# Kernel optimization log

Hardware: AMD Instinct MI355X
Metric: run time of the kernel (lower is better)

Reference implementation:

```python
import jax, jax.numpy as jnp
import numpy as np

CLIP_LEN = 8      # == num_frame
NUM_NODES = 7     # == group_size
NUM_BASIC = 1024
NUM_MIXED = 8192
T = 2 * CLIP_LEN - 1          # 15 temporal offsets
N = 1 + NUM_NODES * CLIP_LEN  # 57 graph size


def setup_inputs() -> dict:
    key = jax.random.key(0)
    k1, k2, k3, k4 = jax.random.split(key, 4)
    mat = jax.random.normal(k1, (NUM_BASIC, NUM_NODES, NUM_NODES), dtype=jnp.float32)
    temp_extent = jax.random.normal(k2, (NUM_BASIC, T), dtype=jnp.float32)
    # nn.Linear(num_basic, num_mixed): weight [out,in], bias [out]
    W = jax.random.normal(k3, (NUM_MIXED, NUM_BASIC), dtype=jnp.float32) * (1.0 / np.sqrt(NUM_BASIC))
    b = jax.random.normal(k4, (NUM_MIXED,), dtype=jnp.float32) * 0.01
    return {"mat": mat, "temp_extent": temp_extent, "W": W, "b": b}


def reference(mat, temp_extent, W, b):
    n, cl = NUM_NODES, CLIP_LEN
    Hb = mat.shape[0]
    te = jax.nn.sigmoid(temp_extent) + 1.0                      # [Hb, T]
    x = jnp.einsum('ht,hnm->htmn', te, mat)                     # [Hb, T, n, n]
    x = jax.nn.relu(x)
    x = jnp.transpose(x, (1, 2, 3, 0)).reshape(T * n, n, Hb)    # (t m) n h
    y = x @ W.T + b                                             # [(t m), n, Hm]
    y = jax.nn.relu(jnp.transpose(y, (2, 1, 0)))                # [Hm, n, T*n]
    Hm = y.shape[0]
    # vectorized version of the per-frame slice-write loop:
    # frame i reads cols n*(cl-1-i) : n*(2*cl-1-i) of y
    starts = n * (cl - 1 - jnp.arange(cl))                      # [cl]
    idx = starts[:, None] + jnp.arange(n * cl)[None, :]         # [cl, n*cl]
    blocks = y[:, :, idx]                                       # [Hm, n, cl, n*cl]
    blocks = jnp.transpose(blocks, (0, 2, 1, 3)).reshape(Hm, n * cl, n * cl)
    base = jnp.zeros((Hm, N, N), dtype=y.dtype)
    base = base.at[:, 0::7, 0::7].set(1.0)                      # person-node anchors
    mixed = base.at[:, 1:, 1:].set(blocks)                      # [Hm, N, N]
    # degree normalization D^{-1/2} A D^{-1/2} (row sums, clamped at 1)
    d = jnp.clip(mixed.sum(axis=2), 1.0, None) ** -0.5          # [Hm, N]
    ret = d[:, :, None] * mixed * d[:, None, :]
    return ret
```

## Files before the change

### kernel.cpp

```cpp
#include <hip/hip_runtime.h>
#include <hip/hip_bf16.h>

#define HB 1024
#define HM 8192
#define NR 735
#define NPAD 768
#define NOUT 57
#define KSPLIT 2
#define JB 4
#define YS 737

typedef __attribute__((ext_vector_type(8))) _Float16 half8;
typedef __attribute__((ext_vector_type(4))) _Float16 half4v;
typedef __attribute__((ext_vector_type(4))) float floatx4;

__global__ __launch_bounds__(256) void prep_x2_kernel(
    const float* __restrict__ mat, const float* __restrict__ tex,
    _Float16* __restrict__ Xh) {
  const int r = blockIdx.x;
  const int n = r % 7;
  const int tm = r / 7;
  const int m = tm % 7;
  const int t = tm / 7;
#pragma unroll
  for (int i = 0; i < 4; ++i) {
    const int h = i * 256 + threadIdx.x;
    float v = 0.f;
    if (r < NR) {
      const float mv = mat[h * 49 + n * 7 + m];
      const float te = 1.f / (1.f + expf(-tex[h * 15 + t])) + 1.f;
      v = te * mv;
      v = v > 0.f ? v : 0.f;
    }
    Xh[r * HB + h] = (_Float16)v;
  }
}

__global__ __launch_bounds__(256, 3) void gemm_kernel(
    const float* __restrict__ W,
    const _Float16* __restrict__ Xh,
    _Float16* __restrict__ Yp) {
  __shared__ __align__(16) _Float16 As[128 * 32];
  __shared__ __align__(16) _Float16 Bs[128 * 32];

  const int tid = threadIdx.x;
  const int lane = tid & 63;
  const int wave = tid >> 6;
  const int bn = blockIdx.x;
  const int bm = blockIdx.y;
  const int ks = blockIdx.z;
  const int wm = (wave >> 1) * 64;
  const int wn = (wave & 1) * 64;

  floatx4 acc[4][4] = {};

  const int brow = lane >> 2;
  const int bkh = (lane & 3) * 8;
  const size_t bbase = (size_t)(bn * 128) * HB;

  const int arow = tid >> 3;
  const int acol = (tid & 7) * 4;
  const float* const Wbase = W + (size_t)(bm * 128) * HB;

  const int mrow = lane & 15;
  const int quad = lane >> 4;

  const int kbeg = ks * (HB / KSPLIT);
  for (int kk = 0; kk < HB / KSPLIT; kk += 32) {
    const int k0 = kbeg + kk;
#pragma unroll
    for (int it = 0; it < 2; ++it) {
      const int chunk = wave * 2 + it;
      __builtin_amdgcn_global_load_lds(
          (const __attribute__((address_space(1))) void*)(
              Xh + bbase + (size_t)(chunk * 16 + brow) * HB + k0 + bkh),
          (__attribute__((address_space(3))) void*)(Bs + chunk * 512), 16, 0, 0);
    }
#pragma unroll
    for (int it = 0; it < 4; ++it) {
      const int r = it * 32 + arow;
      const float4 w4 = *(const float4*)(Wbase + (size_t)r * HB + k0 + acol);
      half4v h4;
      h4.x = (_Float16)w4.x;
      h4.y = (_Float16)w4.y;
      h4.z = (_Float16)w4.z;
      h4.w = (_Float16)w4.w;
      *(half4v*)(As + r * 32 + acol) = h4;
    }
    __syncthreads();

    half8 af[4], bf[4];
#pragma unroll
    for (int i = 0; i < 4; ++i) {
      af[i] = *(const half8*)(As + (wm + i * 16 + mrow) * 32 + quad * 8);
      bf[i] = *(const half8*)(Bs + (wn + i * 16 + mrow) * 32 + quad * 8);
    }
#pragma unroll
    for (int i = 0; i < 4; ++i)
#pragma unroll
      for (int j = 0; j < 4; ++j)
        acc[i][j] = __builtin_amdgcn_mfma_f32_16x16x32_f16(af[i], bf[j], acc[i][j], 0, 0, 0);
    __syncthreads();
  }

  _Float16* const Yk = Yp + (size_t)ks * HM * NPAD;
#pragma unroll
  for (int i = 0; i < 4; ++i) {
#pragma unroll
    for (int j = 0; j < 4; ++j) {
#pragma unroll
      for (int reg = 0; reg < 4; ++reg) {
        const int grow = bm * 128 + wm + i * 16 + quad * 4 + reg;
        const int gcol = bn * 128 + wn + j * 16 + mrow;
        Yk[(size_t)grow * NPAD + gcol] = (_Float16)acc[i][j][reg];
      }
    }
  }
}

__global__ __launch_bounds__(256) void epilogue_kernel(
    const _Float16* __restrict__ Yp, const float* __restrict__ bias,
    float* __restrict__ out) {
  const int tid = threadIdx.x;
  const int j0 = blockIdx.x * JB;
  __shared__ float ly[JB][YS];
  __shared__ float dd[JB][NOUT];

#pragma unroll
  for (int jj = 0; jj < JB; ++jj) {
    const _Float16* y0 = Yp + (size_t)(j0 + jj) * NPAD;
    const _Float16* y1 = Yp + (size_t)(HM + j0 + jj) * NPAD;
    const float bj = bias[j0 + jj];
    for (int i = tid; i < NR; i += 256) {
      float v = (float)y0[i] + (float)y1[i] + bj;
      ly[jj][i] = v > 0.f ? v : 0.f;
    }
  }
  __syncthreads();

  if (tid < JB * NOUT) {
    const int jj = tid / NOUT;
    const int r = tid % NOUT;
    float s;
    if (r == 0) {
      s = 9.f;
    } else {
      const int c = (r - 1) / 7;
      const int n = (r - 1) % 7;
      const int base = 7 * (7 - c);
      s = (n == 6) ? 1.f : 0.f;
#pragma unroll
      for (int p = 0; p < 56; ++p) s += ly[jj][(base + p) * 7 + n];
    }
    s = s < 1.f ? 1.f : s;
    dd[jj][r] = rsqrtf(s);
  }
  __syncthreads();

  float4* const o4 = (float4*)(out + (size_t)j0 * (NOUT * NOUT));
  for (int idx = tid; idx < NOUT * NOUT; idx += 256) {
    float4 v4;
#pragma unroll
    for (int e = 0; e < 4; ++e) {
      const int g = idx * 4 + e;
      const int jj = g / (NOUT * NOUT);
      const int i = g % (NOUT * NOUT);
      const int r = i / NOUT;
      const int q = i % NOUT;
      float v;
      if (r == 0) {
        v = (q % 7 == 0) ? dd[jj][0] * dd[jj][q] : 0.f;
      } else {
        const int c = (r - 1) / 7;
        const int n = (r - 1) % 7;
        if (q == 0)
          v = (n == 6) ? dd[jj][r] * dd[jj][0] : 0.f;
        else
          v = dd[jj][r] * ly[jj][(7 * (7 - c) + q - 1) * 7 + n] * dd[jj][q];
      }
      ((float*)&v4)[e] = v;
    }
    o4[idx] = v4;
  }
}

extern "C" void kernel_launch(void* const* d_in, const int* in_sizes, int n_in,
                              void* d_out, int out_size, void* d_ws, size_t ws_size,
                              hipStream_t stream) {
  const float* mat = (const float*)d_in[0];
  const float* tex = (const float*)d_in[1];
  const float* W = (const float*)d_in[2];
  const float* b = (const float*)d_in[3];
  float* out = (float*)d_out;

  char* ws = (char*)d_ws;
  _Float16* Xh = (_Float16*)ws;
  _Float16* Yp = (_Float16*)(ws + (size_t)NPAD * HB * 2);

  prep_x2_kernel<<<NPAD, 256, 0, stream>>>(mat, tex, Xh);
  gemm_kernel<<<dim3(NPAD / 128, HM / 128, KSPLIT), 256, 0, stream>>>(W, Xh, Yp);
  epilogue_kernel<<<HM / JB, 256, 0, stream>>>(Yp, b, out);
}
```

Baseline: 194.0 us.

## Pre-convert W to fp16, stage GEMM output through LDS, vectorize epilogue loads

The fp32 weight matrix is now converted to fp16 in a separate pass inside the prep kernel, so the GEMM can stream both operands with direct global-to-LDS loads instead of converting W per tile. The GEMM output is transposed through shared memory so it is written as 16-byte row chunks rather than scattered 2-byte stores. The epilogue reads the partial sums with half8 vector loads. This adds a full extra read and write of W (about 32MB plus 16MB) every call, which may cost more than the per-tile conversion it replaces, even though the GEMM re-reads W six times.

```diff
diff --git a/kernel.cpp b/kernel.cpp
--- a/kernel.cpp
+++ b/kernel.cpp
@@ -8,40 +8,56 @@
 #define NOUT 57
 #define KSPLIT 2
 #define JB 4
-#define YS 737
+#define YS 740
+#define CTS 132
 
 typedef __attribute__((ext_vector_type(8))) _Float16 half8;
 typedef __attribute__((ext_vector_type(4))) _Float16 half4v;
 typedef __attribute__((ext_vector_type(4))) float floatx4;
 
-__global__ __launch_bounds__(256) void prep_x2_kernel(
+__global__ __launch_bounds__(256) void prep_kernel(
     const float* __restrict__ mat, const float* __restrict__ tex,
-    _Float16* __restrict__ Xh) {
-  const int r = blockIdx.x;
-  const int n = r % 7;
-  const int tm = r / 7;
-  const int m = tm % 7;
-  const int t = tm / 7;
-#pragma unroll
-  for (int i = 0; i < 4; ++i) {
-    const int h = i * 256 + threadIdx.x;
-    float v = 0.f;
-    if (r < NR) {
-      const float mv = mat[h * 49 + n * 7 + m];
-      const float te = 1.f / (1.f + expf(-tex[h * 15 + t])) + 1.f;
-      v = te * mv;
-      v = v > 0.f ? v : 0.f;
-    }
-    Xh[r * HB + h] = (_Float16)v;
+    const float4* __restrict__ W4, _Float16* __restrict__ Xh,
+    half4v* __restrict__ Wh4) {
+  const int bid = blockIdx.x;
+  if (bid < NPAD) {
+    const int r = bid;
+    const int n = r % 7;
+    const int tm = r / 7;
+    const int m = tm % 7;
+    const int t = tm / 7;
+#pragma unroll
+    for (int i = 0; i < 4; ++i) {
+      const int h = i * 256 + threadIdx.x;
+      float v = 0.f;
+      if (r < NR) {
+        const float mv = mat[h * 49 + n * 7 + m];
+        const float te = 1.f / (1.f + expf(-tex[h * 15 + t])) + 1.f;
+        v = te * mv;
+        v = v > 0.f ? v : 0.f;
+      }
+      Xh[r * HB + h] = (_Float16)v;
+    }
+  } else {
+    const int idx = (bid - NPAD) * 256 + threadIdx.x;
+    const float4 v = W4[idx];
+    half4v h;
+    h.x = (_Float16)v.x;
+    h.y = (_Float16)v.y;
+    h.z = (_Float16)v.z;
+    h.w = (_Float16)v.w;
+    Wh4[idx] = h;
   }
 }
 
 __global__ __launch_bounds__(256, 3) void gemm_kernel(
-    const float* __restrict__ W,
-    const _Float16* __restrict__ Xh,
+    const _Float16* __restrict__ A,
+    const _Float16* __restrict__ B,
     _Float16* __restrict__ Yp) {
-  __shared__ __align__(16) _Float16 As[128 * 32];
-  __shared__ __align__(16) _Float16 Bs[128 * 32];
+  __shared__ __align__(16) _Float16 smem[64 * CTS];
+  _Float16* const As = smem;
+  _Float16* const Bs = smem + 4096;
+  _Float16* const Ct = smem;
 
   const int tid = threadIdx.x;
   const int lane = tid & 63;
@@ -54,13 +70,10 @@
 
   floatx4 acc[4][4] = {};
 
-  const int brow = lane >> 2;
-  const int bkh = (lane & 3) * 8;
+  const int srow = lane >> 2;
+  const int skh = (lane & 3) * 8;
+  const size_t abase = (size_t)(bm * 128) * HB;
   const size_t bbase = (size_t)(bn * 128) * HB;
-
-  const int arow = tid >> 3;
-  const int acol = (tid & 7) * 4;
-  const float* const Wbase = W + (size_t)(bm * 128) * HB;
 
   const int mrow = lane & 15;
   const int quad = lane >> 4;
@@ -71,21 +84,13 @@
 #pragma unroll
     for (int it = 0; it < 2; ++it) {
       const int chunk = wave * 2 + it;
+      const int row = chunk * 16 + srow;
       __builtin_amdgcn_global_load_lds(
-          (const __attribute__((address_space(1))) void*)(
-              Xh + bbase + (size_t)(chunk * 16 + brow) * HB + k0 + bkh),
+          (const __attribute__((address_space(1))) void*)(A + abase + (size_t)row * HB + k0 + skh),
+          (__attribute__((address_space(3))) void*)(As + chunk * 512), 16, 0, 0);
+      __builtin_amdgcn_global_load_lds(
+          (const __attribute__((address_space(1))) void*)(B + bbase + (size_t)row * HB + k0 + skh),
           (__attribute__((address_space(3))) void*)(Bs + chunk * 512), 16, 0, 0);
-    }
-#pragma unroll
-    for (int it = 0; it < 4; ++it) {
-      const int r = it * 32 + arow;
-      const float4 w4 = *(const float4*)(Wbase + (size_t)r * HB + k0 + acol);
-      half4v h4;
-      h4.x = (_Float16)w4.x;
-      h4.y = (_Float16)w4.y;
-      h4.z = (_Float16)w4.z;
-      h4.w = (_Float16)w4.w;
-      *(half4v*)(As + r * 32 + acol) = h4;
     }
     __syncthreads();
 
@@ -105,16 +110,27 @@
 
   _Float16* const Yk = Yp + (size_t)ks * HM * NPAD;
 #pragma unroll
-  for (int i = 0; i < 4; ++i) {
-#pragma unroll
-    for (int j = 0; j < 4; ++j) {
-#pragma unroll
-      for (int reg = 0; reg < 4; ++reg) {
-        const int grow = bm * 128 + wm + i * 16 + quad * 4 + reg;
-        const int gcol = bn * 128 + wn + j * 16 + mrow;
-        Yk[(size_t)grow * NPAD + gcol] = (_Float16)acc[i][j][reg];
-      }
-    }
+  for (int half = 0; half < 2; ++half) {
+    if ((wave >> 1) == half) {
+#pragma unroll
+      for (int i = 0; i < 4; ++i)
+#pragma unroll
+        for (int j = 0; j < 4; ++j)
+#pragma unroll
+          for (int reg = 0; reg < 4; ++reg)
+            Ct[(i * 16 + quad * 4 + reg) * CTS + wn + j * 16 + mrow] =
+                (_Float16)acc[i][j][reg];
+    }
+    __syncthreads();
+#pragma unroll
+    for (int s = 0; s < 4; ++s) {
+      const int cid = s * 256 + tid;
+      const int row = cid >> 4;
+      const int c8 = cid & 15;
+      const half8 v = *(const half8*)(Ct + row * CTS + c8 * 8);
+      *(half8*)(Yk + (size_t)(bm * 128 + half * 64 + row) * NPAD + bn * 128 + c8 * 8) = v;
+    }
+    __syncthreads();
   }
 }
 
@@ -126,15 +142,25 @@
   __shared__ float ly[JB][YS];
   __shared__ float dd[JB][NOUT];
 
-#pragma unroll
-  for (int jj = 0; jj < JB; ++jj) {
-    const _Float16* y0 = Yp + (size_t)(j0 + jj) * NPAD;
-    const _Float16* y1 = Yp + (size_t)(HM + j0 + jj) * NPAD;
+  for (int idx = tid; idx < JB * 92; idx += 256) {
+    const int jj = idx / 92;
+    const int c8 = idx % 92;
+    const half8 a = *(const half8*)(Yp + (size_t)(j0 + jj) * NPAD + c8 * 8);
+    const half8 b2 = *(const half8*)(Yp + (size_t)(HM + j0 + jj) * NPAD + c8 * 8);
     const float bj = bias[j0 + jj];
-    for (int i = tid; i < NR; i += 256) {
-      float v = (float)y0[i] + (float)y1[i] + bj;
-      ly[jj][i] = v > 0.f ? v : 0.f;
-    }
+    float4 lo, hi;
+#pragma unroll
+    for (int e = 0; e < 4; ++e) {
+      float v = (float)a[e] + (float)b2[e] + bj;
+      ((float*)&lo)[e] = v > 0.f ? v : 0.f;
+    }
+#pragma unroll
+    for (int e = 0; e < 4; ++e) {
+      float v = (float)a[4 + e] + (float)b2[4 + e] + bj;
+      ((float*)&hi)[e] = v > 0.f ? v : 0.f;
+    }
+    *(float4*)(&ly[jj][c8 * 8]) = lo;
+    *(float4*)(&ly[jj][c8 * 8 + 4]) = hi;
   }
   __syncthreads();
 
@@ -195,9 +221,11 @@
 
   char* ws = (char*)d_ws;
   _Float16* Xh = (_Float16*)ws;
-  _Float16* Yp = (_Float16*)(ws + (size_t)NPAD * HB * 2);
-
-  prep_x2_kernel<<<NPAD, 256, 0, stream>>>(mat, tex, Xh);
-  gemm_kernel<<<dim3(NPAD / 128, HM / 128, KSPLIT), 256, 0, stream>>>(W, Xh, Yp);
+  _Float16* Wh = (_Float16*)(ws + (size_t)NPAD * HB * 2);
+  _Float16* Yp = (_Float16*)(ws + (size_t)(NPAD + HM) * HB * 2);
+
+  prep_kernel<<<NPAD + HM * HB / 4 / 256, 256, 0, stream>>>(
+      mat, tex, (const float4*)W, Xh, (half4v*)Wh);
+  gemm_kernel<<<dim3(NPAD / 128, HM / 128, KSPLIT), 256, 0, stream>>>(Wh, Xh, Yp);
   epilogue_kernel<<<HM / JB, 256, 0, stream>>>(Yp, b, out);
 }
```

Result: faster. 189.8 us (-2.2%).
